# Optimization experiments

Hardware: AMD Instinct MI355X
Metric: run time of the kernel (lower is better)

## Reference

```python
import jax, jax.numpy as jnp
import numpy as np

H_DIM_EXP = 25  # n = 2**25 = 33,554,432

def setup_inputs() -> dict:
    key = jax.random.key(0)
    x = jax.random.normal(key, (2 ** H_DIM_EXP,), dtype=jnp.float32)
    return {"x": x, "h_dim_exp": H_DIM_EXP}

def reference(x, h_dim_exp):
    # Fast Walsh-Hadamard transform. The original views x as [1,2,2,...,2,1]
    # and applies a (+,-) butterfly along each of the log2(n) axes-of-size-2.
    # Butterfly stages on distinct bits commute, so we process bits from low
    # to high with rank-3 reshapes instead of a rank-(exp+2) tensor.
    y = x
    for i in range(h_dim_exp):
        y = y.reshape(-1, 2, 2 ** i)        # (n/2^{i+1}, 2, 2^i)
        a, b = y[:, 0, :], y[:, 1, :]
        y = jnp.stack([a + b, a - b], axis=1)
    return y.reshape(x.shape)
```

## Files before the change

### kernel.cpp

```cpp
#include <hip/hip_runtime.h>


typedef float vf4 __attribute__((ext_vector_type(4)));

__device__ __forceinline__ float4 ntload(const float4* p) {
  vf4 r = __builtin_nontemporal_load(reinterpret_cast<const vf4*>(p));
  return *reinterpret_cast<float4*>(&r);
}

__device__ __forceinline__ void bfly(float4& a, float4& b) {
  float ax = a.x, ay = a.y, az = a.z, aw = a.w;
  a.x = ax + b.x; a.y = ay + b.y; a.z = az + b.z; a.w = aw + b.w;
  b.x = ax - b.x; b.y = ay - b.y; b.z = az - b.z; b.w = aw - b.w;
}

__device__ __forceinline__ void cross4(float4 (&v)[16]) {
#pragma unroll
  for (int m = 0; m < 4; ++m) {
#pragma unroll
    for (int k = 0; k < 16; ++k) {
      if (!(k & (1 << m))) bfly(v[k], v[k | (1 << m)]);
    }
  }
}

__device__ __forceinline__ void cross3(float4 (&v)[8]) {
#pragma unroll
  for (int m = 0; m < 3; ++m) {
#pragma unroll
    for (int k = 0; k < 8; ++k) {
      if (!(k & (1 << m))) bfly(v[k], v[k | (1 << m)]);
    }
  }
}

__global__ __launch_bounds__(512) void wht_pass1(const float4* __restrict__ in4,
                                                 float4* __restrict__ out4) {
  __shared__ float4 lds[4096];
  const int t = threadIdx.x;
  const int base4 = (int)blockIdx.x << 12;
  float4 v[8];
#pragma unroll
  for (int k = 0; k < 8; ++k)
    v[k] = ntload(&in4[base4 + t + (k << 9)]);
#pragma unroll
  for (int k = 0; k < 8; ++k) {
    float4 a = v[k];
    float s0 = a.x + a.y, d0 = a.x - a.y, s1 = a.z + a.w, d1 = a.z - a.w;
    v[k].x = s0 + s1; v[k].y = d0 + d1; v[k].z = s0 - s1; v[k].w = d0 - d1;
  }
  cross3(v);

#pragma unroll
  for (int k = 0; k < 8; ++k) { int s = t + (k << 9); lds[s ^ ((s >> 3) & 7)] = v[k]; }
  __syncthreads();
#pragma unroll
  for (int u = 0; u < 8; ++u) { int s = u + (t << 3); v[u] = lds[s ^ ((s >> 3) & 7)]; }
  cross3(v);

#pragma unroll
  for (int u = 0; u < 8; ++u) { int s = u + (t << 3); lds[s ^ ((s >> 3) & 7)] = v[u]; }
  __syncthreads();
  {
    const int c0 = t & 7, c1 = t >> 3;
#pragma unroll
    for (int u = 0; u < 8; ++u) {
      int s = c0 + (u << 3) + (c1 << 6);
      v[u] = lds[s ^ ((s >> 3) & 7)];
    }
  }
  cross3(v);

  {
    const int c0 = t & 7, c1 = t >> 3;
#pragma unroll
    for (int u = 0; u < 8; ++u) {
      int s = c0 + (u << 3) + (c1 << 6);
      lds[s ^ ((s >> 3) & 7)] = v[u];
    }
  }
  __syncthreads();
  const int c0b = t & 63, c1b = t >> 6;
#pragma unroll
  for (int u = 0; u < 8; ++u) {
    int s = c0b + (u << 6) + (c1b << 9);
    v[u] = lds[s ^ ((s >> 3) & 7)];
  }
  cross3(v);

#pragma unroll
  for (int u = 0; u < 8; ++u) out4[base4 + c0b + (u << 6) + (c1b << 9)] = v[u];
}

__global__ __launch_bounds__(1024, 4) void wht_pass2(float4* __restrict__ b4) {
  __shared__ float4 lds[4096];
  const int t = threadIdx.x;
  const int cb4 = (int)blockIdx.x << 3;
  const int c4 = t & 7;
  const int cc = t & 1;
  const int qt = (t >> 1) & 3;
  const int rlo = t >> 3;
  float4 v[16];
#pragma unroll
  for (int k = 0; k < 16; ++k)
    v[k] = b4[((long)(rlo + (k << 7)) << 12) + cb4 + c4];
  cross4(v);

#pragma unroll 1
  for (int r4 = 0; r4 < 4; ++r4) {
    __syncthreads();
    if (qt == r4) {
#pragma unroll
      for (int k = 0; k < 16; ++k) {
        int q = ((rlo + (k << 7)) << 1) | cc;
        lds[q ^ (((q >> 8) & 3) << 1)] = v[k];
      }
    }
    __syncthreads();
    if (qt == r4) {
#pragma unroll
      for (int rb = 0; rb < 16; ++rb) {
        int q = ((rb + (rlo << 4)) << 1) | cc;
        v[rb] = lds[q ^ (((q >> 8) & 3) << 1)];
      }
    }
  }
  cross4(v);

  const int rlowC = (t >> 3) & 15;
  const int rhi4C = (t & 1) | (((t >> 7) & 7) << 1);
#pragma unroll 1
  for (int r4 = 0; r4 < 4; ++r4) {
    __syncthreads();
    if (qt == r4) {
#pragma unroll
      for (int rb = 0; rb < 16; ++rb) {
        int q = ((rb + (rlo << 4)) << 1) | cc;
        lds[q ^ (((q >> 8) & 3) << 1)] = v[rb];
      }
    }
    __syncthreads();
    if (qt == r4) {
#pragma unroll
      for (int i = 0; i < 16; ++i) {
        int rm = i & 7, c = i >> 3;
        int r = rlowC + (rm << 4) + (rhi4C << 7);
        int q = (r << 1) | c;
        v[i] = lds[q ^ (((q >> 8) & 3) << 1)];
      }
    }
  }
#pragma unroll
  for (int m = 0; m < 3; ++m) {
#pragma unroll
    for (int i = 0; i < 16; ++i) {
      if (!(i & (1 << m))) bfly(v[i], v[i | (1 << m)]);
    }
  }

#pragma unroll
  for (int i = 0; i < 16; ++i) {
    int rm = i & 7, c = i >> 3;
    int r = rlowC + (rm << 4) + (rhi4C << 7);
    b4[((long)r << 12) + cb4 + (qt << 1) + c] = v[i];
  }
}

extern "C" void kernel_launch(void* const* d_in, const int* in_sizes, int n_in,
                              void* d_out, int out_size, void* d_ws, size_t ws_size,
                              hipStream_t stream) {
  (void)in_sizes; (void)n_in; (void)d_ws; (void)ws_size; (void)out_size;
  const float* x = (const float*)d_in[0];
  float* out = (float*)d_out;
  wht_pass1<<<2048, 512, 0, stream>>>((const float4*)x, (float4*)out);
  wht_pass2<<<512, 1024, 0, stream>>>((float4*)out);
}
```

Baseline: 296.6 us.

## Remap pass2 LDS exchanges so final stores write full contiguous column chunks

Reworks the thread-to-element mapping of the two LDS transpose rounds in the second pass. Each thread now ends up owning the same 8-float4 column slice it loaded, so the final global stores are coalesced across c4 and are issued as nontemporal stores. The first sync of the first round is skipped, and index math switches from 64-bit to 32-bit. The new bit-permuted LDS addresses drop the XOR swizzle, which risks more bank conflicts.

```diff
diff --git a/kernel.cpp b/kernel.cpp
--- a/kernel.cpp
+++ b/kernel.cpp
@@ -6,6 +6,10 @@
 __device__ __forceinline__ float4 ntload(const float4* p) {
   vf4 r = __builtin_nontemporal_load(reinterpret_cast<const vf4*>(p));
   return *reinterpret_cast<float4*>(&r);
+}
+__device__ __forceinline__ void ntstore(float4* p, float4 v) {
+  __builtin_nontemporal_store(*reinterpret_cast<vf4*>(&v),
+                              reinterpret_cast<vf4*>(p));
 }
 
 __device__ __forceinline__ void bfly(float4& a, float4& b) {
@@ -97,72 +101,66 @@
   const int t = threadIdx.x;
   const int cb4 = (int)blockIdx.x << 3;
   const int c4 = t & 7;
-  const int cc = t & 1;
-  const int qt = (t >> 1) & 3;
-  const int rlo = t >> 3;
+  const int rA = t >> 3;
+  const int g1 = (t >> 8) & 3;
+  const int g2 = (t >> 6) & 3;
   float4 v[16];
 #pragma unroll
   for (int k = 0; k < 16; ++k)
-    v[k] = b4[((long)(rlo + (k << 7)) << 12) + cb4 + c4];
+    v[k] = b4[((rA + (k << 7)) << 12) + cb4 + c4];
   cross4(v);
 
+  const int e1w = (t & 63) | (((t >> 7) & 1) << 6) | (((t >> 6) & 1) << 11);
+  const int e1r = (t & 7) | (((t >> 3) & 1) << 6) | (((t >> 4) & 3) << 7) |
+                  (((t >> 6) & 1) << 9) | (((t >> 7) & 1) << 10);
 #pragma unroll 1
-  for (int r4 = 0; r4 < 4; ++r4) {
-    __syncthreads();
-    if (qt == r4) {
+  for (int q = 0; q < 4; ++q) {
+    if (q) __syncthreads();
+    if (g1 == q) {
 #pragma unroll
-      for (int k = 0; k < 16; ++k) {
-        int q = ((rlo + (k << 7)) << 1) | cc;
-        lds[q ^ (((q >> 8) & 3) << 1)] = v[k];
-      }
+      for (int k = 0; k < 16; ++k)
+        lds[e1w | ((k & 3) << 7) | (((k >> 2) & 1) << 9) | ((k >> 3) << 10)] = v[k];
     }
     __syncthreads();
-    if (qt == r4) {
+    if (g1 == q) {
 #pragma unroll
-      for (int rb = 0; rb < 16; ++rb) {
-        int q = ((rb + (rlo << 4)) << 1) | cc;
-        v[rb] = lds[q ^ (((q >> 8) & 3) << 1)];
-      }
+      for (int j = 0; j < 16; ++j)
+        v[j] = lds[e1r | ((j & 7) << 3) | ((j >> 3) << 11)];
     }
   }
   cross4(v);
 
-  const int rlowC = (t >> 3) & 15;
-  const int rhi4C = (t & 1) | (((t >> 7) & 7) << 1);
+  const int e2w = (t & 7) | (((t >> 3) & 1) << 6) | (((t >> 4) & 3) << 7) |
+                  (((t >> 8) & 1) << 9) | (((t >> 9) & 1) << 10);
+  const int e2r = (t & 63) | (((t >> 8) & 3) << 7);
 #pragma unroll 1
-  for (int r4 = 0; r4 < 4; ++r4) {
+  for (int q = 0; q < 4; ++q) {
     __syncthreads();
-    if (qt == r4) {
+    if (g2 == q) {
 #pragma unroll
-      for (int rb = 0; rb < 16; ++rb) {
-        int q = ((rb + (rlo << 4)) << 1) | cc;
-        lds[q ^ (((q >> 8) & 3) << 1)] = v[rb];
-      }
+      for (int j = 0; j < 16; ++j)
+        lds[e2w | ((j & 7) << 3) | ((j >> 3) << 11)] = v[j];
     }
     __syncthreads();
-    if (qt == r4) {
+    if (g2 == q) {
 #pragma unroll
-      for (int i = 0; i < 16; ++i) {
-        int rm = i & 7, c = i >> 3;
-        int r = rlowC + (rm << 4) + (rhi4C << 7);
-        int q = (r << 1) | c;
-        v[i] = lds[q ^ (((q >> 8) & 3) << 1)];
-      }
+      for (int i = 0; i < 16; ++i)
+        v[i] = lds[e2r | (((i >> 1) & 1) << 6) | (((i >> 2) & 1) << 9) |
+                   ((i >> 3) << 10) | ((i & 1) << 11)];
     }
   }
 #pragma unroll
-  for (int m = 0; m < 3; ++m) {
+  for (int m = 1; m < 4; ++m) {
 #pragma unroll
-    for (int i = 0; i < 16; ++i) {
+    for (int i = 0; i < 16; ++i)
       if (!(i & (1 << m))) bfly(v[i], v[i | (1 << m)]);
-    }
   }
 
+  const int rstore = ((t >> 3) & 7) | (((t >> 8) & 3) << 7) | (((t >> 6) & 3) << 9);
 #pragma unroll
   for (int i = 0; i < 16; ++i) {
-    int rm = i & 7, c = i >> 3;
-    int r = rlowC + (rm << 4) + (rhi4C << 7);
-    b4[((long)r << 12) + cb4 + (qt << 1) + c] = v[i];
+    int r = rstore | ((i & 1) << 3) | (((i >> 1) & 7) << 4);
+    ntstore(&b4[(r << 12) + cb4 + c4], v[i]);
   }
 }
 
```

After: 273.2 us. -7.9%, faster.
